# Optimization experiments

Measured on AMD Instinct MI355X. Metric: run time of the kernel, lower is better.

## Reference

```python
import jax, jax.numpy as jnp
import numpy as np

NR, NS, TAU, GW = 32, 64, 0.1, 0.5
NEG = jnp.float32(-1e30)

def _nrm(x):
    return x / jnp.maximum(jnp.linalg.norm(x, axis=-1, keepdims=True), 1e-12)

def _pair_loss(fb, ub, am, nm, ra, rp, rn):
    # fb [HW,D] features, ub [HW] uncertainty, am/nm [HW] bool anchor(=pos)/neg masks,
    # ra/rp/rn [HW] uniform random scores standing in for torch.randperm.
    def sel(mask, r, k):  # random subset of size k from mask (invalid slots flagged)
        _, idx = jax.lax.top_k(jnp.where(mask, r, NEG), k)
        return idx, mask[idx]
    def hard(mask, r):  # randperm[:2*Ns] then topk Ns by uncertainty
        cidx, cval = sel(mask, r, 2 * NS)
        _, t = jax.lax.top_k(jnp.where(cval, ub[cidx], NEG), NS)
        return cidx[t], cval[t]
    aidx, aval = sel(am, ra, NR)
    pidx, pval = hard(am, rp)
    nidx, nval = hard(nm, rn)
    q  = _nrm(fb[aidx])   # [NR,D]
    P  = _nrm(fb[pidx])   # [NS,D]
    Ng = _nrm(fb[nidx])   # [NS,D]
    pw = pval.astype(fb.dtype)[:, None]
    nw = nval.astype(fb.dtype)[:, None]
    p = (jnp.exp(P @ q.T / TAU) * pw).sum(0)   # [NR]
    n = (jnp.exp(Ng @ q.T / TAU) * nw).sum(0)  # [NR]
    inc = (am.sum() >= 1) & (nm.sum() >= 1)
    p = p + (1.0 - inc.astype(p.dtype))  # safe when excluded
    per = -jnp.log(p / (p + n + 1e-8))
    af = aval.astype(per.dtype)
    bl = (per * af).sum() / jnp.maximum(af.sum(), 1.0)
    return jnp.where(inc, bl, 0.0), inc

def _forward(feat, labels, prob_ori, prob_aug, unc, r_anc, r_pos, r_neg,
             w1, b1, gamma, beta, w2, b2):
    B, D, H, W = feat.shape
    # proj: 1x1 conv -> BN (training stats) -> relu -> 1x1 conv
    x = jnp.einsum('bdhw,ed->behw', feat, w1) + b1[None, :, None, None]
    mu = x.mean((0, 2, 3), keepdims=True)
    var = x.var((0, 2, 3), keepdims=True)
    x = gamma[None, :, None, None] * (x - mu) / jnp.sqrt(var + 1e-5) + beta[None, :, None, None]
    x = jax.nn.relu(x)
    proj = jnp.einsum('bdhw,ed->behw', x, w2) + b2[None, :, None, None]

    rel = prob_ori.argmax(1) == prob_aug.argmax(1)
    diff = unc > 0.5
    valid = (rel & diff).reshape(B, -1)
    lab = labels.reshape(B, -1)
    f = proj.transpose(0, 2, 3, 1).reshape(B, -1, D)
    uf = unc.reshape(B, -1)
    m1 = valid & (lab == 1)
    m0 = valid & (lab == 0)

    # ---- local loss: classes (1 vs 0) and (0 vs 1) ----
    anc = jnp.stack([m1, m0], 1)  # [B,2,HW]
    neg = jnp.stack([m0, m1], 1)
    pair = jax.vmap(jax.vmap(_pair_loss, in_axes=(None, None, 0, 0, 0, 0, 0)),
                    in_axes=(0, 0, 0, 0, 0, 0, 0))
    bl, inc = pair(f, uf, anc, neg, r_anc, r_pos, r_neg)
    l_local = bl.sum() / jnp.maximum(inc.sum(), 1)

    # ---- global loss with sequential memory bank (bank starts empty) ----
    fgf = m1.astype(f.dtype); bgf = m0.astype(f.dtype)
    cf = fgf.sum(1); cb = bgf.sum(1)
    m_fg = (f * fgf[..., None]).sum(1) / jnp.maximum(cf, 1.0)[:, None]
    m_bg = (f * bgf[..., None]).sum(1) / jnp.maximum(cb, 1.0)[:, None]
    vg = (cf >= 1) & (cb >= 1)
    qf, qb = _nrm(m_fg), _nrm(m_bg)
    # bank content at step b: prototypes of valid j <= b (detached)
    M = ((jnp.arange(B)[None, :] <= jnp.arange(B)[:, None]) & vg[None, :]).astype(f.dtype)  # [b,j]
    Sf = jnp.exp(jax.lax.stop_gradient(qb) @ qf.T / TAU)  # [j,b]
    Sb = jnp.exp(jax.lax.stop_gradient(qf) @ qb.T / TAU)
    nf = jnp.einsum('jb,bj->b', Sf, M)
    nb = jnp.einsum('jb,bj->b', Sb, M)
    pf = jnp.exp((qf * qf).sum(-1) / TAU)
    pb = jnp.exp((qb * qb).sum(-1) / TAU)
    lg = -jnp.log(pf / (pf + nf + 1e-8)) - jnp.log(pb / (pb + nb + 1e-8))
    l_global = (vg.astype(f.dtype) * lg).sum() / jnp.maximum(vg.sum(), 1)

    return l_local + GW * l_global, l_local, l_global

def setup_inputs() -> dict:
    key = jax.random.key(0)
    ks = jax.random.split(key, 16)
    B, D, H, W = 4, 256, 128, 128
    HW = H * W
    return {
        'feat': jax.random.normal(ks[0], (B, D, H, W), jnp.float32),
        'labels': jax.random.randint(ks[1], (B, H, W), 0, 2, jnp.int32),
        'prob_ori': jax.random.uniform(ks[2], (B, 2, H, W), jnp.float32),
        'prob_aug': jax.random.uniform(ks[3], (B, 2, H, W), jnp.float32),
        'unc': jax.random.uniform(ks[4], (B, H, W), jnp.float32),
        'r_anc': jax.random.uniform(ks[5], (B, 2, HW), jnp.float32),
        'r_pos': jax.random.uniform(ks[6], (B, 2, HW), jnp.float32),
        'r_neg': jax.random.uniform(ks[7], (B, 2, HW), jnp.float32),
        'w1': jax.random.normal(ks[8], (D, D), jnp.float32) * 0.05,
        'b1': jnp.zeros((D,), jnp.float32),
        'gamma': jnp.ones((D,), jnp.float32),
        'beta': jnp.zeros((D,), jnp.float32),
        'w2': jax.random.normal(ks[9], (D, D), jnp.float32) * 0.05,
        'b2': jnp.zeros((D,), jnp.float32),
    }

def reference(feat, labels, prob_ori, prob_aug, unc, r_anc, r_pos, r_neg,
              w1, b1, gamma, beta, w2, b2):
    return _forward(feat, labels, prob_ori, prob_aug, unc, r_anc, r_pos, r_neg,
                    w1, b1, gamma, beta, w2, b2)
```

## Files before the change

### kernel.cpp

```cpp
#include <hip/hip_runtime.h>
#include <hip/hip_bf16.h>
#include <float.h>
#include <math.h>

#define HW 16384
#define NBATCH 4
#define DIM 256
#define NEGV (-1e30f)
#define NPP 160

#define OFF_CHAN_SUM 0
#define OFF_CHAN_SQ  1024
#define OFF_MEAN     2048
#define OFF_ISTD     3072
#define OFF_S1       4096
#define OFF_S0       8192
#define OFF_CF       12288
#define OFF_CB       12304
#define OFF_BL       12320
#define OFF_INCF     12352
#define OFF_PPCNT    12416
#define OFF_QBUF     16384
#define OFF_BCNT     24576
#define OFF_MCLS     40960
#define OFF_SELIDX   303104
#define OFF_SELW     308224
#define OFF_ROWS     313344
#define OFF_W1T      1624064
#define OFF_RAW      1886208
#define OFF_CKEYS_XL 68995072
#define WS_NEED_FAST 68995072ull
#define WS_NEED_XL   72140800ull

#define NSEL 24

__device__ __forceinline__ unsigned f2mono(float f) {
  unsigned u = __float_as_uint(f);
  return (u & 0x80000000u) ? ~u : (u | 0x80000000u);
}

__device__ __forceinline__ void sort_desc(unsigned long long* sk, int* si, int n, int tid) {
  for (int ksz = 2; ksz <= n; ksz <<= 1) {
    for (int j = ksz >> 1; j > 0; j >>= 1) {
      __syncthreads();
      if (tid < n) {
        int ixj = tid ^ j;
        if (ixj > tid) {
          unsigned long long a = sk[tid], b = sk[ixj];
          bool up = (tid & ksz) == 0;
          if (up ? (a < b) : (a > b)) {
            sk[tid] = b; sk[ixj] = a;
            int t2 = si[tid]; si[tid] = si[ixj]; si[ixj] = t2;
          }
        }
      }
    }
  }
  __syncthreads();
}

__global__ __launch_bounds__(256) void k_maskc2(
    const float* __restrict__ po, const float* __restrict__ pa,
    const float* __restrict__ unc, const int* __restrict__ lab,
    const float* __restrict__ r_anc, const float* __restrict__ r_pos,
    const float* __restrict__ r_neg, const float* __restrict__ w1,
    int* __restrict__ mcls, int* __restrict__ bcnt,
    unsigned long long* __restrict__ ckeys, float* __restrict__ w1T,
    float* __restrict__ chanSum, float* __restrict__ chanSq,
    float* __restrict__ S1, float* __restrict__ S0,
    int* __restrict__ ppcnt) {
  __shared__ int lcnt[24];
  int tid = threadIdx.x;
  int g = blockIdx.x * 256 + tid;
  int b = g >> 14;
  int lb = blockIdx.x & 63;
  int i = g & (HW - 1);
  if (tid < 24) lcnt[tid] = 0;
  __syncthreads();
  float o0 = po[(size_t)(b*2+0)*HW + i];
  float o1 = po[(size_t)(b*2+1)*HW + i];
  float a0 = pa[(size_t)(b*2+0)*HW + i];
  float a1 = pa[(size_t)(b*2+1)*HW + i];
  bool rel = ((o1 > o0) == (a1 > a0));
  bool valid = rel && (unc[g] > 0.5f);
  int l = lab[g];
  int cls = valid ? ((l == 1) ? 1 : 2) : 0;
  mcls[g] = cls;
  int t0 = 0, t1 = 0, t2 = 0, loc0 = 0, loc1 = 0, loc2 = 0;
  unsigned long long k0 = 0, k1 = 0, k2 = 0;
  if (cls) {
    int co = cls - 1;
    unsigned idxf = (unsigned)(16383 - i);
    t0 = (b*2 + co)*3 + 0;
    t1 = (b*2 + co)*3 + 1;
    t2 = (b*2 + (1 - co))*3 + 2;
    k0 = ((unsigned long long)f2mono(r_anc[(size_t)(b*2 + co)*HW + i]) << 14) | idxf;
    k1 = ((unsigned long long)f2mono(r_pos[(size_t)(b*2 + co)*HW + i]) << 14) | idxf;
    k2 = ((unsigned long long)f2mono(r_neg[(size_t)(b*2 + (1 - co))*HW + i]) << 14) | idxf;
    loc0 = atomicAdd(&lcnt[t0], 1);
    loc1 = atomicAdd(&lcnt[t1], 1);
    loc2 = atomicAdd(&lcnt[t2], 1);
  }
  __syncthreads();
  if (tid < 24 && (tid / 6) == b)
    bcnt[tid*64 + lb] = lcnt[tid];
  if (cls) {
    ckeys[(size_t)t0*HW + lb*256 + loc0] = k0;
    ckeys[(size_t)t1*HW + lb*256 + loc1] = k1;
    ckeys[(size_t)t2*HW + lb*256 + loc2] = k2;
  }
  if (blockIdx.x < 16) {
    int d0 = blockIdx.x * 16;
    float v[16];
    #pragma unroll
    for (int j = 0; j < 16; ++j) v[j] = w1[(size_t)tid*DIM + d0 + j];
    #pragma unroll
    for (int j = 0; j < 16; ++j) w1T[(size_t)(d0 + j)*DIM + tid] = v[j];
  }
  if (blockIdx.x == 16) { chanSum[tid] = 0.f; chanSq[tid] = 0.f; }
  if (blockIdx.x == 17) {
    #pragma unroll
    for (int j = 0; j < 4; ++j) S1[j*256 + tid] = 0.f;
  }
  if (blockIdx.x == 18) {
    #pragma unroll
    for (int j = 0; j < 4; ++j) S0[j*256 + tid] = 0.f;
  }
  if (blockIdx.x == 19 && tid == 0) *ppcnt = 0;
}

__device__ void selc_body(const int* __restrict__ bcnt,
                          const unsigned long long* __restrict__ ckeys,
                          const float* __restrict__ unc,
                          int* __restrict__ selIdx, float* __restrict__ selW,
                          int* __restrict__ cf, int* __restrict__ cb,
                          int task, int tid, char* sh) {
  unsigned long long* sk = (unsigned long long*)sh;
  int* si    = (int*)(sh + 1024);
  int* cIdx  = (int*)(sh + 1536);
  int* hist  = (int*)(sh + 2048);
  int* sufs  = (int*)(sh + 3072);
  int* sbcnt = (int*)(sh + 4096);
  unsigned char* cVal = (unsigned char*)(sh + 4352);
  int* scal  = (int*)(sh + 4480);

  int pair = task / 3, which = task % 3;
  int b = pair >> 1, c = pair & 1;
  const unsigned long long* keys = ckeys + (size_t)task * HW;
  if (tid < 64) sbcnt[tid] = bcnt[task*64 + tid];
  __syncthreads();
  if (tid == 0) { int s = 0; for (int i2 = 0; i2 < 64; ++i2) s += sbcnt[i2]; scal[3] = s; }
  __syncthreads();
  int cnt = scal[3];
  if (which == 0 && tid == 0) { if (c == 0) cf[b] = cnt; else cb[b] = cnt; }
  int K1 = (which == 0) ? 32 : 128;
  int outBase = pair*NPP + (which == 0 ? 0 : (which == 1 ? 32 : 96));

  int mseg = tid >> 2;
  int msub = tid & 3;
  int mcnt = sbcnt[mseg];
  const unsigned long long* mkeys = keys + mseg*256;

  unsigned long long pref = 0;
  if (cnt > K1) {
    const int shifts[6]  = {38, 30, 22, 14, 6, 0};
    const int bitsArr[6] = { 8,  8,  8,  8, 8, 6};
    int k = K1;
    for (int p = 0; p < 6; ++p) {
      int shift = shifts[p], nbits = bitsArr[p], nb = 1 << nbits;
      hist[tid] = 0;
      __syncthreads();
      for (int pos = msub; pos < mcnt; pos += 4) {
        unsigned long long key = mkeys[pos];
        if ((key >> (shift + nbits)) == pref)
          atomicAdd(&hist[(int)((key >> shift) & (nb - 1))], 1);
      }
      __syncthreads();
      if (tid < nb) sufs[tid] = hist[tid];
      __syncthreads();
      for (int off = 1; off < nb; off <<= 1) {
        int add = 0;
        if (tid < nb && tid + off < nb) add = sufs[tid + off];
        __syncthreads();
        if (tid < nb) sufs[tid] += add;
        __syncthreads();
      }
      if (tid < nb) {
        int sthis = sufs[tid];
        int snext = (tid + 1 < nb) ? sufs[tid + 1] : 0;
        if (sthis >= k && snext < k) { scal[0] = tid; scal[1] = k - snext; }
      }
      __syncthreads();
      pref = (pref << nbits) | (unsigned)scal[0];
      k = scal[1];
      __syncthreads();
    }
  }

  if (tid == 0) scal[2] = 0;
  __syncthreads();
  for (int pos = msub; pos < mcnt; pos += 4) {
    unsigned long long key = mkeys[pos];
    if (key >= pref) {
      int p2 = atomicAdd(&scal[2], 1);
      if (p2 < 128) { sk[p2] = key; si[p2] = 16383 - (int)(key & 16383); }
    }
  }
  __syncthreads();
  int gcnt = scal[2];
  if (tid < K1 && tid >= gcnt) { sk[tid] = 0ull; si[tid] = 0; }

  sort_desc(sk, si, K1, tid);

  if (which == 0) {
    if (tid < 32) {
      selIdx[outBase + tid] = si[tid];
      selW[outBase + tid]   = (sk[tid] != 0ull) ? 1.f : 0.f;
    }
    return;
  }

  if (tid < 128) {
    cIdx[tid] = si[tid];
    cVal[tid] = (sk[tid] != 0ull) ? 1 : 0;
  }
  __syncthreads();
  if (tid < 128) {
    float u2 = cVal[tid] ? unc[(size_t)b*HW + cIdx[tid]] : NEGV;
    sk[tid] = ((unsigned long long)f2mono(u2) << 7) | (unsigned)(127 - tid);
    si[tid] = tid;
  }
  sort_desc(sk, si, 128, tid);
  if (tid < 64) {
    int t = si[tid];
    selIdx[outBase + tid] = cIdx[t];
    selW[outBase + tid]   = cVal[t] ? 1.f : 0.f;
  }
}

__global__ __launch_bounds__(256) void k_selc2(
    const int* __restrict__ bcnt, const unsigned long long* __restrict__ ckeys,
    const float* __restrict__ unc,
    int* __restrict__ selIdx, float* __restrict__ selW,
    int* __restrict__ cf, int* __restrict__ cb) {
  __shared__ __align__(16) char sh[4608];
  selc_body(bcnt, ckeys, unc, selIdx, selW, cf, cb, blockIdx.x, threadIdx.x, sh);
}

#define BK 32
#define LDA 132

__device__ void mm8_body(
    const float* __restrict__ feat, const float* __restrict__ w1T,
    const int* __restrict__ mcls,
    float* __restrict__ chanSum, float* __restrict__ chanSq,
    float* __restrict__ rawout, int bid, int tid, float* smem) {
  float* As = smem;
  float* Bs = smem + BK*LDA;
  int ct = bid & 1;
  int rt = bid >> 1;
  int b  = rt >> 7;
  int i0 = (rt & 127) << 7;
  int c0 = ct << 7;
  int tx = tid & 15, ty = tid >> 4;
  float acc[8][8];
  #pragma unroll
  for (int r = 0; r < 8; ++r)
    #pragma unroll
    for (int c = 0; c < 8; ++c) acc[r][c] = 0.f;

  for (int kc = 0; kc < 8; ++kc) {
    int d0 = kc * BK;
    #pragma unroll
    for (int it = 0; it < 4; ++it) {
      int e = it*1024 + tid*4;
      int k = e >> 7, r = e & 127;
      float4 v = *(const float4*)&feat[((size_t)(b*DIM + d0 + k))*HW + i0 + r];
      *(float4*)&As[k*LDA + r] = v;
    }
    #pragma unroll
    for (int it = 0; it < 4; ++it) {
      int e = it*1024 + tid*4;
      int k = e >> 7, c = e & 127;
      float4 v = *(const float4*)&w1T[(size_t)(d0 + k)*DIM + c0 + c];
      *(float4*)&Bs[k*LDA + c] = v;
    }
    __syncthreads();
    #pragma unroll
    for (int k = 0; k < BK; ++k) {
      float4 a0 = *(const float4*)&As[k*LDA + ty*4];
      float4 a1 = *(const float4*)&As[k*LDA + 64 + ty*4];
      float4 b0 = *(const float4*)&Bs[k*LDA + tx*4];
      float4 b1 = *(const float4*)&Bs[k*LDA + 64 + tx*4];
      float ar[8] = {a0.x,a0.y,a0.z,a0.w, a1.x,a1.y,a1.z,a1.w};
      float bc[8] = {b0.x,b0.y,b0.z,b0.w, b1.x,b1.y,b1.z,b1.w};
      #pragma unroll
      for (int r = 0; r < 8; ++r)
        #pragma unroll
        for (int c = 0; c < 8; ++c)
          acc[r][c] += ar[r]*bc[c];
    }
    __syncthreads();
  }

  float* pS = smem;
  float* pQ = smem + 2048;
  #pragma unroll
  for (int c = 0; c < 8; ++c) {
    int lcol = (c < 4) ? (tx*4 + c) : (64 + tx*4 + (c - 4));
    float s = 0.f, q = 0.f;
    #pragma unroll
    for (int r = 0; r < 8; ++r) { float v = acc[r][c]; s += v; q += v*v; }
    pS[ty*128 + lcol] = s;
    pQ[ty*128 + lcol] = q;
  }
  __syncthreads();
  if (tid < 128) {
    float s = 0.f, q = 0.f;
    #pragma unroll
    for (int t2 = 0; t2 < 16; ++t2) { s += pS[t2*128 + tid]; q += pQ[t2*128 + tid]; }
    atomicAdd(&chanSum[c0 + tid], s);
    atomicAdd(&chanSq[c0 + tid],  q);
  }

  #pragma unroll
  for (int r = 0; r < 8; ++r) {
    int lrow = (r < 4) ? (ty*4 + r) : (64 + ty*4 + (r - 4));
    int g = rt*128 + lrow;
    if (mcls[g] != 0) {
      float4 lo; lo.x = acc[r][0]; lo.y = acc[r][1]; lo.z = acc[r][2]; lo.w = acc[r][3];
      float4 hi; hi.x = acc[r][4]; hi.y = acc[r][5]; hi.z = acc[r][6]; hi.w = acc[r][7];
      *(float4*)&rawout[(size_t)g*DIM + c0 + tx*4]      = lo;
      *(float4*)&rawout[(size_t)g*DIM + c0 + 64 + tx*4] = hi;
    }
  }
}

__global__ __launch_bounds__(256) void k_mmsel(
    const float* __restrict__ feat, const float* __restrict__ w1T,
    const int* __restrict__ mcls,
    float* __restrict__ chanSum, float* __restrict__ chanSq,
    float* __restrict__ rawout,
    const int* __restrict__ bcnt, const unsigned long long* __restrict__ ckeys,
    const float* __restrict__ unc,
    int* __restrict__ selIdx, float* __restrict__ selW,
    int* __restrict__ cf, int* __restrict__ cb, int nSel) {
  __shared__ __align__(16) float smem[2*BK*LDA];
  int bid = blockIdx.x;
  if (bid < nSel)
    selc_body(bcnt, ckeys, unc, selIdx, selW, cf, cb, bid, threadIdx.x, (char*)smem);
  else
    mm8_body(feat, w1T, mcls, chanSum, chanSq, rawout, bid - nSel, threadIdx.x, smem);
}

__global__ __launch_bounds__(256) void k_post(
    const float* __restrict__ raw, const int* __restrict__ mcls,
    const float* __restrict__ chanSum, const float* __restrict__ chanSq,
    const float* __restrict__ gamma, const float* __restrict__ beta,
    const float* __restrict__ w2, const float* __restrict__ b2,
    const int* __restrict__ selIdx, const float* __restrict__ selW,
    float* __restrict__ S1, float* __restrict__ S0,
    float* __restrict__ rows) {
  __shared__ __align__(16) float sh[2048];
  const float nconst = (float)(NBATCH * HW);
  int tid = threadIdx.x;

  if (blockIdx.x < 256) {
    float* p1 = sh;
    float* p2 = sh + 1024;
    int w = tid >> 6, lane = tid & 63;
    int p0 = blockIdx.x << 8;
    int b = p0 >> 14;
    int ch = lane*4;
    float4 G = *(const float4*)&gamma[ch];
    float4 Bt = *(const float4*)&beta[ch];
    float4 CS = *(const float4*)&chanSum[ch];
    float4 CQ = *(const float4*)&chanSq[ch];
    float m0 = CS.x/nconst, m1 = CS.y/nconst, m2 = CS.z/nconst, m3 = CS.w/nconst;
    float v0 = CQ.x/nconst - m0*m0, v1 = CQ.y/nconst - m1*m1;
    float v2 = CQ.z/nconst - m2*m2, v3 = CQ.w/nconst - m3*m3;
    float i0 = 1.0f/sqrtf(v0 + 1e-5f), i1 = 1.0f/sqrtf(v1 + 1e-5f);
    float i2 = 1.0f/sqrtf(v2 + 1e-5f), i3 = 1.0f/sqrtf(v3 + 1e-5f);
    float A0 = G.x*i0, A1 = G.y*i1, A2 = G.z*i2, A3 = G.w*i3;
    float s1[4] = {0,0,0,0}, s0[4] = {0,0,0,0};
    int g0 = p0 + w*64;
    for (int t = 0; t < 64; ++t) {
      int g = g0 + t;
      int cls = mcls[g];
      if (cls == 0) continue;
      float4 v = *(const float4*)&raw[(size_t)g*DIM + ch];
      float r0 = A0*(v.x - m0) + Bt.x; r0 = r0 > 0.f ? r0 : 0.f;
      float r1 = A1*(v.y - m1) + Bt.y; r1 = r1 > 0.f ? r1 : 0.f;
      float r2 = A2*(v.z - m2) + Bt.z; r2 = r2 > 0.f ? r2 : 0.f;
      float r3 = A3*(v.w - m3) + Bt.w; r3 = r3 > 0.f ? r3 : 0.f;
      if (cls == 1) { s1[0]+=r0; s1[1]+=r1; s1[2]+=r2; s1[3]+=r3; }
      else          { s0[0]+=r0; s0[1]+=r1; s0[2]+=r2; s0[3]+=r3; }
    }
    #pragma unroll
    for (int j = 0; j < 4; ++j) {
      p1[w*256 + ch + j] = s1[j];
      p2[w*256 + ch + j] = s0[j];
    }
    __syncthreads();
    float a = p1[tid] + p1[256+tid] + p1[512+tid] + p1[768+tid];
    float d = p2[tid] + p2[256+tid] + p2[512+tid] + p2[768+tid];
    atomicAdd(&S1[b*DIM + tid], a);
    atomicAdd(&S0[b*DIM + tid], d);
  } else {
    float* rl  = sh;
    float* red = sh + 1024;
    int blk = blockIdx.x - 256;
    int slot0 = blk * 4;
    int pair = slot0 / NPP;
    int b = pair >> 1;
    int e = tid;
    float m = chanSum[e] / nconst;
    float v = chanSq[e] / nconst - m*m;
    float istd = 1.0f / sqrtf(v + 1e-5f);
    float A = gamma[e]*istd;
    float Bt = beta[e];
    bool ok[4];
    #pragma unroll
    for (int s = 0; s < 4; ++s) {
      int slot = slot0 + s;
      ok[s] = (selW[slot] != 0.f);
      float rv = 0.f;
      if (ok[s]) {
        int i = selIdx[slot];
        float acc = raw[((size_t)b*HW + i)*DIM + e];
        float bn = A*(acc - m) + Bt;
        rv = bn > 0.f ? bn : 0.f;
      }
      rl[s*256 + e] = rv;
    }
    __syncthreads();
    float b2e = b2[e];
    float pj[4] = {b2e, b2e, b2e, b2e};
    const float4* w4 = (const float4*)&w2[(size_t)e*DIM];
    #pragma unroll 8
    for (int d4 = 0; d4 < DIM/4; ++d4) {
      float4 w = w4[d4];
      #pragma unroll
      for (int s = 0; s < 4; ++s) {
        float4 a = *(const float4*)&rl[s*256 + d4*4];
        pj[s] += a.x*w.x + a.y*w.y + a.z*w.z + a.w*w.w;
      }
    }
    #pragma unroll
    for (int s = 0; s < 4; ++s) red[s*256 + e] = pj[s]*pj[s];
    __syncthreads();
    for (int off = 128; off > 0; off >>= 1) {
      if (e < off) {
        #pragma unroll
        for (int s = 0; s < 4; ++s) red[s*256 + e] += red[s*256 + e + off];
      }
      __syncthreads();
    }
    #pragma unroll
    for (int s = 0; s < 4; ++s) {
      float sc = 1.f / fmaxf(sqrtf(red[s*256]), 1e-12f);
      rows[(size_t)(slot0 + s)*DIM + e] = ok[s] ? pj[s]*sc : 0.f;
    }
  }
}

__device__ void pair_body(
    const float* __restrict__ rows, const float* __restrict__ selW,
    const int* __restrict__ cf, const int* __restrict__ cb,
    float* __restrict__ BL, float* __restrict__ INCF, int pair, int tid) {
  __shared__ float q[32*257];
  __shared__ float pacc[256], nacc[256];
  __shared__ float red[64];
  int b = pair >> 1, c = pair & 1;
  for (int l = tid; l < 32*DIM; l += 256) {
    int r = l >> 8, d = l & 255;
    q[r*257 + d] = rows[((size_t)pair*NPP + r)*DIM + d];
  }
  __syncthreads();
  int g = tid >> 5, r = tid & 31;
  float ap = 0.f, an = 0.f;
  for (int so = 0; so < 8; ++so) {
    int s = so*8 + g;
    const float* Pr = &rows[((size_t)pair*NPP + 32 + s)*DIM];
    const float* Nr = &rows[((size_t)pair*NPP + 96 + s)*DIM];
    float dp = 0.f, dn = 0.f;
    for (int d = 0; d < DIM; ++d) {
      float qv = q[r*257 + d];
      dp += Pr[d]*qv;
      dn += Nr[d]*qv;
    }
    ap += expf(dp*10.f) * selW[pair*NPP + 32 + s];
    an += expf(dn*10.f) * selW[pair*NPP + 96 + s];
  }
  pacc[tid] = ap; nacc[tid] = an;
  __syncthreads();
  if (tid < 32) {
    float p = 0.f, n = 0.f;
    for (int gg = 0; gg < 8; ++gg) { p += pacc[gg*32 + tid]; n += nacc[gg*32 + tid]; }
    int amC = (c == 0) ? cf[b] : cb[b];
    int nmC = (c == 0) ? cb[b] : cf[b];
    bool inc = (amC >= 1) && (nmC >= 1);
    if (!inc) p += 1.f;
    float per = -logf(p / (p + n + 1e-8f));
    float af = selW[pair*NPP + tid];
    red[tid]      = per*af;
    red[32 + tid] = af;
  }
  __syncthreads();
  if (tid == 0) {
    float s = 0.f, sa = 0.f;
    for (int rr = 0; rr < 32; ++rr) { s += red[rr]; sa += red[32+rr]; }
    int amC = (c == 0) ? cf[b] : cb[b];
    int nmC = (c == 0) ? cb[b] : cf[b];
    bool inc = (amC >= 1) && (nmC >= 1);
    float bl = s / fmaxf(sa, 1.f);
    BL[pair]   = inc ? bl : 0.f;
    INCF[pair] = inc ? 1.f : 0.f;
  }
}

__device__ void proto_body(
    const float* __restrict__ S1, const float* __restrict__ S0,
    const int* __restrict__ cf, const int* __restrict__ cb,
    const float* __restrict__ w2, const float* __restrict__ b2,
    float* __restrict__ qbuf, int idx, int l) {
  int b = idx >> 1, side = idx & 1;
  const float* S = (side == 0) ? &S1[b*DIM] : &S0[b*DIM];
  float cnt = (float)((side == 0) ? cf[b] : cb[b]);
  float m[4]; float n2p = 0.f;
  #pragma unroll
  for (int k = 0; k < 4; ++k) {
    int e = l + 64*k;
    float acc = 0.f;
    const float* w2r = &w2[(size_t)e*DIM];
    for (int d = 0; d < DIM; ++d) acc += S[d]*w2r[d];
    float mv = (acc + cnt*b2[e]) / fmaxf(cnt, 1.f);
    m[k] = mv; n2p += mv*mv;
  }
  #pragma unroll
  for (int off = 32; off > 0; off >>= 1) n2p += __shfl_down(n2p, off, 64);
  float n2 = __shfl(n2p, 0, 64);
  float sc = 1.f / fmaxf(sqrtf(n2), 1e-12f);
  #pragma unroll
  for (int k = 0; k < 4; ++k)
    qbuf[(size_t)(side*4 + b)*DIM + l + 64*k] = m[k]*sc;
}

__device__ void glob_body(
    const float* __restrict__ qbuf,
    const int* __restrict__ cf, const int* __restrict__ cb,
    const float* __restrict__ BL, const float* __restrict__ INCF,
    float* __restrict__ out, int l) {
  float qf[4][4], qb[4][4];
  #pragma unroll
  for (int b = 0; b < 4; ++b)
    #pragma unroll
    for (int k = 0; k < 4; ++k) {
      qf[b][k] = qbuf[(size_t)b*DIM + l + 64*k];
      qb[b][k] = qbuf[(size_t)(4 + b)*DIM + l + 64*k];
    }
  float pd[24];
  #pragma unroll
  for (int j = 0; j < 4; ++j)
    #pragma unroll
    for (int b = 0; b < 4; ++b) {
      float s = 0.f;
      #pragma unroll
      for (int k = 0; k < 4; ++k) s += qb[j][k]*qf[b][k];
      pd[j*4 + b] = s;
    }
  #pragma unroll
  for (int b = 0; b < 4; ++b) {
    float s1 = 0.f, s2 = 0.f;
    #pragma unroll
    for (int k = 0; k < 4; ++k) { s1 += qf[b][k]*qf[b][k]; s2 += qb[b][k]*qb[b][k]; }
    pd[16 + b] = s1; pd[20 + b] = s2;
  }
  #pragma unroll
  for (int t = 0; t < 24; ++t)
    #pragma unroll
    for (int off = 32; off > 0; off >>= 1)
      pd[t] += __shfl_down(pd[t], off, 64);
  if (l == 0) {
    bool vg[4]; float vgs = 0.f;
    for (int b = 0; b < 4; ++b) {
      vg[b] = (cf[b] >= 1) && (cb[b] >= 1);
      if (vg[b]) vgs += 1.f;
    }
    float gsum = 0.f;
    for (int b = 0; b < 4; ++b) {
      float nf = 0.f, nb = 0.f;
      for (int j = 0; j <= b; ++j) if (vg[j]) {
        nf += expf(10.f*pd[j*4 + b]);
        nb += expf(10.f*pd[b*4 + j]);
      }
      float pf = expf(10.f*pd[16 + b]);
      float pb = expf(10.f*pd[20 + b]);
      float lg = -logf(pf/(pf + nf + 1e-8f)) - logf(pb/(pb + nb + 1e-8f));
      if (vg[b]) gsum += lg;
    }
    float l_global = gsum / fmaxf(vgs, 1.f);
    float bls = 0.f, incs = 0.f;
    for (int p = 0; p < 8; ++p) { bls += BL[p]; incs += INCF[p]; }
    float l_local = bls / fmaxf(incs, 1.f);
    out[0] = l_local + 0.5f*l_global;
    out[1] = l_local;
    out[2] = l_global;
  }
}

__global__ __launch_bounds__(256) void k_pp(
    const float* __restrict__ rows, const float* __restrict__ selW,
    const int* __restrict__ cf, const int* __restrict__ cb,
    float* __restrict__ BL, float* __restrict__ INCF,
    const float* __restrict__ S1, const float* __restrict__ S0,
    const float* __restrict__ w2, const float* __restrict__ b2,
    float* __restrict__ qbuf, int* __restrict__ ppcnt,
    float* __restrict__ out) {
  __shared__ int isLast;
  if (blockIdx.x < 8) {
    pair_body(rows, selW, cf, cb, BL, INCF, blockIdx.x, threadIdx.x);
  } else {
    if (threadIdx.x < 64)
      proto_body(S1, S0, cf, cb, w2, b2, qbuf, blockIdx.x - 8, threadIdx.x);
  }
  __syncthreads();
  __threadfence();
  if (threadIdx.x == 0) isLast = (atomicAdd(ppcnt, 1) == 15);
  __syncthreads();
  if (isLast) {
    __threadfence();
    if (threadIdx.x < 64)
      glob_body(qbuf, cf, cb, BL, INCF, out, threadIdx.x);
  }
}

__global__ void k_mask(const float* __restrict__ po, const float* __restrict__ pa,
                       const float* __restrict__ unc, const int* __restrict__ lab,
                       int* __restrict__ mcls, int* __restrict__ cf, int* __restrict__ cb) {
  int g = blockIdx.x * 256 + threadIdx.x;
  int b = g >> 14;
  int i = g & (HW - 1);
  float o0 = po[(size_t)(b*2+0)*HW + i];
  float o1 = po[(size_t)(b*2+1)*HW + i];
  float a0 = pa[(size_t)(b*2+0)*HW + i];
  float a1 = pa[(size_t)(b*2+1)*HW + i];
  bool rel = ((o1 > o0) == (a1 > a0));
  bool valid = rel && (unc[g] > 0.5f);
  int l = lab[g];
  int cls = valid ? ((l == 1) ? 1 : 2) : 0;
  mcls[g] = cls;
  if (cls == 1) atomicAdd(&cf[b], 1);
  if (cls == 2) atomicAdd(&cb[b], 1);
}

template<int MODE>
__global__ __launch_bounds__(256) void k_matmul(
    const float* __restrict__ feat, const float* __restrict__ w1,
    float* __restrict__ chanSum, float* __restrict__ chanSq,
    const float* __restrict__ meanr, const float* __restrict__ istd,
    const float* __restrict__ gamma, const float* __restrict__ beta,
    const int* __restrict__ mcls,
    float* __restrict__ S1, float* __restrict__ S0) {
  __shared__ __align__(16) float As[64*68];
  __shared__ __align__(16) float Bs[64*68];
  __shared__ float cA[64], cB[64];
  int tid = threadIdx.x;
  int rt = blockIdx.x;
  int ct = blockIdx.y;
  int b  = rt >> 8;
  int i0 = (rt & 255) << 6;
  int c0 = ct << 6;
  int tx = tid & 15, ty = tid >> 4;
  float acc[4][4] = {{0.f,0.f,0.f,0.f},{0.f,0.f,0.f,0.f},{0.f,0.f,0.f,0.f},{0.f,0.f,0.f,0.f}};
  for (int kc = 0; kc < 4; ++kc) {
    int d0 = kc << 6;
    #pragma unroll
    for (int it = 0; it < 4; ++it) {
      int k  = it*16 + (tid >> 4);
      int rq = tid & 15;
      float4 v = *(const float4*)&feat[((size_t)(b*DIM + d0 + k))*HW + i0 + rq*4];
      *(float4*)&As[k*68 + rq*4] = v;
    }
    #pragma unroll
    for (int it = 0; it < 4; ++it) {
      int col = it*16 + (tid >> 4);
      int kq  = tid & 15;
      float4 v = *(const float4*)&w1[(size_t)(c0 + col)*DIM + d0 + kq*4];
      Bs[(kq*4+0)*68 + col] = v.x;
      Bs[(kq*4+1)*68 + col] = v.y;
      Bs[(kq*4+2)*68 + col] = v.z;
      Bs[(kq*4+3)*68 + col] = v.w;
    }
    __syncthreads();
    #pragma unroll
    for (int k = 0; k < 64; ++k) {
      float4 av = *(const float4*)&As[k*68 + ty*4];
      float4 bv = *(const float4*)&Bs[k*68 + tx*4];
      float aa[4] = {av.x, av.y, av.z, av.w};
      float bb[4] = {bv.x, bv.y, bv.z, bv.w};
      #pragma unroll
      for (int rr = 0; rr < 4; ++rr)
        #pragma unroll
        for (int cc = 0; cc < 4; ++cc)
          acc[rr][cc] += aa[rr]*bb[cc];
    }
    __syncthreads();
  }
  if (tid < 64) { cA[tid] = 0.f; cB[tid] = 0.f; }
  __syncthreads();
  if (MODE == 0) {
    float s[4] = {0,0,0,0}, q[4] = {0,0,0,0};
    #pragma unroll
    for (int rr = 0; rr < 4; ++rr)
      #pragma unroll
      for (int cc = 0; cc < 4; ++cc) { float v = acc[rr][cc]; s[cc] += v; q[cc] += v*v; }
    #pragma unroll
    for (int cc = 0; cc < 4; ++cc) {
      atomicAdd(&cA[tx*4+cc], s[cc]);
      atomicAdd(&cB[tx*4+cc], q[cc]);
    }
    __syncthreads();
    if (tid < 64) {
      atomicAdd(&chanSum[c0 + tid], cA[tid]);
      atomicAdd(&chanSq[c0 + tid],  cB[tid]);
    }
  } else {
    float A[4], M[4], Bt[4];
    #pragma unroll
    for (int cc = 0; cc < 4; ++cc) {
      int c = c0 + tx*4 + cc;
      A[cc] = gamma[c]*istd[c]; M[cc] = meanr[c]; Bt[cc] = beta[c];
    }
    float s1[4] = {0,0,0,0}, s0[4] = {0,0,0,0};
    #pragma unroll
    for (int rr = 0; rr < 4; ++rr) {
      int g = rt*64 + ty*4 + rr;
      int cls = mcls[g];
      if (cls == 0) continue;
      #pragma unroll
      for (int cc = 0; cc < 4; ++cc) {
        float v = A[cc]*(acc[rr][cc] - M[cc]) + Bt[cc];
        v = v > 0.f ? v : 0.f;
        if (cls == 1) s1[cc] += v; else s0[cc] += v;
      }
    }
    #pragma unroll
    for (int cc = 0; cc < 4; ++cc) {
      atomicAdd(&cA[tx*4+cc], s1[cc]);
      atomicAdd(&cB[tx*4+cc], s0[cc]);
    }
    __syncthreads();
    if (tid < 64) {
      atomicAdd(&S1[b*DIM + c0 + tid], cA[tid]);
      atomicAdd(&S0[b*DIM + c0 + tid], cB[tid]);
    }
  }
}

__global__ void k_stats(const float* __restrict__ chanSum, const float* __restrict__ chanSq,
                        float* __restrict__ meanr, float* __restrict__ istd) {
  int e = threadIdx.x;
  const float n = (float)(NBATCH * HW);
  float m = chanSum[e] / n;
  float v = chanSq[e] / n - m*m;
  meanr[e] = m;
  istd[e]  = 1.0f / sqrtf(v + 1e-5f);
}

__global__ __launch_bounds__(256) void k_select(
    const int* __restrict__ mcls,
    const float* __restrict__ r_anc, const float* __restrict__ r_pos, const float* __restrict__ r_neg,
    const float* __restrict__ unc,
    int* __restrict__ selIdx, float* __restrict__ selW) {
  __shared__ int hist[256];
  __shared__ int sufs[256];
  __shared__ unsigned long long sk[128];
  __shared__ int si[128];
  __shared__ int cIdx[128];
  __shared__ unsigned char cVal[128];
  __shared__ int sh_bin, sh_k, gcnt;

  int tid  = threadIdx.x;
  int task = blockIdx.x;
  int pair = task / 3, which = task % 3;
  int b = pair >> 1, c = pair & 1;
  int wantA = (c == 0) ? 1 : 2;
  int want  = (which == 2) ? (3 - wantA) : wantA;
  const int* mc = mcls + (size_t)b * HW;
  const float* r = (which == 0) ? r_anc : (which == 1 ? r_pos : r_neg);
  r += (size_t)(b*2 + c) * HW;

  int K1 = (which == 0) ? 32 : 128;
  int outBase = pair*NPP + (which == 0 ? 0 : (which == 1 ? 32 : 96));

  const int shifts[6]  = {38, 30, 22, 14, 6, 0};
  const int bitsArr[6] = { 8,  8,  8,  8, 8, 6};
  unsigned long long pref = 0;
  int k = K1;
  for (int p = 0; p < 6; ++p) {
    int shift = shifts[p];
    int nbits = bitsArr[p];
    int nb = 1 << nbits;
    hist[tid] = 0;
    __syncthreads();
    int lastBin = -1, lc = 0;
    #pragma unroll 4
    for (int j = 0; j < 64; ++j) {
      int i = tid + j*256;
      float kv = (mc[i] == want) ? r[i] : NEGV;
      unsigned long long key = ((unsigned long long)f2mono(kv) << 14) | (unsigned)(16383 - i);
      if ((key >> (shift + nbits)) == pref) {
        int bin = (int)((key >> shift) & (nb - 1));
        if (bin == lastBin) { ++lc; }
        else {
          if (lastBin >= 0) atomicAdd(&hist[lastBin], lc);
          lastBin = bin; lc = 1;
        }
      }
    }
    if (lastBin >= 0) atomicAdd(&hist[lastBin], lc);
    __syncthreads();
    if (tid < nb) sufs[tid] = hist[tid];
    __syncthreads();
    for (int off = 1; off < nb; off <<= 1) {
      int add = 0;
      if (tid < nb && tid + off < nb) add = sufs[tid + off];
      __syncthreads();
      if (tid < nb) sufs[tid] += add;
      __syncthreads();
    }
    if (tid < nb) {
      int sthis = sufs[tid];
      int snext = (tid + 1 < nb) ? sufs[tid + 1] : 0;
      if (sthis >= k && snext < k) { sh_bin = tid; sh_k = k - snext; }
    }
    __syncthreads();
    pref = (pref << nbits) | (unsigned)sh_bin;
    k = sh_k;
    __syncthreads();
  }

  if (tid == 0) gcnt = 0;
  __syncthreads();
  #pragma unroll 4
  for (int j = 0; j < 64; ++j) {
    int i = tid + j*256;
    float kv = (mc[i] == want) ? r[i] : NEGV;
    unsigned long long key = ((unsigned long long)f2mono(kv) << 14) | (unsigned)(16383 - i);
    if (key >= pref) {
      int p2 = atomicAdd(&gcnt, 1);
      if (p2 < 128) { sk[p2] = key; si[p2] = i; }
    }
  }
  __syncthreads();
  if (tid < K1 && tid >= gcnt) { sk[tid] = 0ull; si[tid] = 0; }

  sort_desc(sk, si, K1, tid);

  if (which == 0) {
    if (tid < 32) {
      selIdx[outBase + tid] = si[tid];
      selW[outBase + tid]   = ((sk[tid] >> 14) >= 0x80000000ull) ? 1.f : 0.f;
    }
    return;
  }

  if (tid < 128) {
    cIdx[tid] = si[tid];
    cVal[tid] = ((sk[tid] >> 14) >= 0x80000000ull) ? 1 : 0;
  }
  __syncthreads();
  if (tid < 128) {
    float u2 = cVal[tid] ? unc[(size_t)b*HW + cIdx[tid]] : NEGV;
    sk[tid] = ((unsigned long long)f2mono(u2) << 7) | (unsigned)(127 - tid);
    si[tid] = tid;
  }
  sort_desc(sk, si, 128, tid);
  if (tid < 64) {
    int t = si[tid];
    selIdx[outBase + tid] = cIdx[t];
    selW[outBase + tid]   = cVal[t] ? 1.f : 0.f;
  }
}

__global__ __launch_bounds__(256) void k_rowproj(
    const float* __restrict__ feat, const float* __restrict__ w1, const float* __restrict__ w2,
    const float* __restrict__ b2, const float* __restrict__ gamma, const float* __restrict__ beta,
    const float* __restrict__ meanr, const float* __restrict__ istd,
    const int* __restrict__ selIdx, float* __restrict__ rows) {
  __shared__ __align__(16) float fr[DIM];
  __shared__ __align__(16) float rl[DIM];
  __shared__ float red[256];
  int slot = blockIdx.x;
  int pair = slot / NPP;
  int b = pair >> 1;
  int i = selIdx[slot];
  int e = threadIdx.x;
  fr[e] = feat[((size_t)(b*DIM + e))*HW + i];
  __syncthreads();
  float acc = 0.f;
  {
    const float4* f4 = (const float4*)fr;
    const float4* w4 = (const float4*)&w1[(size_t)e*DIM];
    #pragma unroll 8
    for (int d = 0; d < DIM/4; ++d) {
      float4 a = f4[d], w = w4[d];
      acc += a.x*w.x + a.y*w.y + a.z*w.z + a.w*w.w;
    }
  }
  float bn = gamma[e]*istd[e]*(acc - meanr[e]) + beta[e];
  rl[e] = bn > 0.f ? bn : 0.f;
  __syncthreads();
  float pj = b2[e];
  {
    const float4* f4 = (const float4*)rl;
    const float4* w4 = (const float4*)&w2[(size_t)e*DIM];
    #pragma unroll 8
    for (int d = 0; d < DIM/4; ++d) {
      float4 a = f4[d], w = w4[d];
      pj += a.x*w.x + a.y*w.y + a.z*w.z + a.w*w.w;
    }
  }
  red[e] = pj*pj;
  __syncthreads();
  for (int off = 128; off > 0; off >>= 1) {
    if (e < off) red[e] += red[e+off];
    __syncthreads();
  }
  float sc = 1.f / fmaxf(sqrtf(red[0]), 1e-12f);
  rows[(size_t)slot*DIM + e] = pj * sc;
}

__global__ __launch_bounds__(256) void k_pair(
    const float* __restrict__ rows, const float* __restrict__ selW,
    const int* __restrict__ cf, const int* __restrict__ cb,
    float* __restrict__ BL, float* __restrict__ INCF) {
  pair_body(rows, selW, cf, cb, BL, INCF, blockIdx.x, threadIdx.x);
}

__global__ __launch_bounds__(64) void k_proto(
    const float* __restrict__ S1, const float* __restrict__ S0,
    const int* __restrict__ cf, const int* __restrict__ cb,
    const float* __restrict__ w2, const float* __restrict__ b2,
    float* __restrict__ qbuf) {
  proto_body(S1, S0, cf, cb, w2, b2, qbuf, blockIdx.x, threadIdx.x);
}

__global__ __launch_bounds__(64) void k_glob(
    const float* __restrict__ qbuf,
    const int* __restrict__ cf, const int* __restrict__ cb,
    const float* __restrict__ BL, const float* __restrict__ INCF,
    float* __restrict__ out) {
  glob_body(qbuf, cf, cb, BL, INCF, out, threadIdx.x);
}

extern "C" void kernel_launch(void* const* d_in, const int* in_sizes, int n_in,
                              void* d_out, int out_size, void* d_ws, size_t ws_size,
                              hipStream_t stream) {
  const float* feat     = (const float*)d_in[0];
  const int*   labels   = (const int*)  d_in[1];
  const float* prob_ori = (const float*)d_in[2];
  const float* prob_aug = (const float*)d_in[3];
  const float* unc      = (const float*)d_in[4];
  const float* r_anc    = (const float*)d_in[5];
  const float* r_pos    = (const float*)d_in[6];
  const float* r_neg    = (const float*)d_in[7];
  const float* w1       = (const float*)d_in[8];
  const float* gamma    = (const float*)d_in[10];
  const float* beta     = (const float*)d_in[11];
  const float* w2       = (const float*)d_in[12];
  const float* b2       = (const float*)d_in[13];

  char* ws = (char*)d_ws;
  float* chanSum = (float*)(ws + OFF_CHAN_SUM);
  float* chanSq  = (float*)(ws + OFF_CHAN_SQ);
  float* meanr   = (float*)(ws + OFF_MEAN);
  float* istd    = (float*)(ws + OFF_ISTD);
  float* S1      = (float*)(ws + OFF_S1);
  float* S0      = (float*)(ws + OFF_S0);
  int*   cf      = (int*)  (ws + OFF_CF);
  int*   cb      = (int*)  (ws + OFF_CB);
  float* BLp     = (float*)(ws + OFF_BL);
  float* INCp    = (float*)(ws + OFF_INCF);
  int*   ppcnt   = (int*)  (ws + OFF_PPCNT);
  float* qbuf    = (float*)(ws + OFF_QBUF);
  int*   bcnt    = (int*)  (ws + OFF_BCNT);
  int*   mclsp   = (int*)  (ws + OFF_MCLS);
  int*   selIdx  = (int*)  (ws + OFF_SELIDX);
  float* selW    = (float*)(ws + OFF_SELW);
  float* rowsbuf = (float*)(ws + OFF_ROWS);
  float* w1T     = (float*)(ws + OFF_W1T);
  float* rawbuf  = (float*)(ws + OFF_RAW);

  if (ws_size >= WS_NEED_FAST) {
    bool xl = (ws_size >= WS_NEED_XL);
    unsigned long long* ckeys = (unsigned long long*)(ws + (xl ? OFF_CKEYS_XL : OFF_RAW));

    k_maskc2<<<256, 256, 0, stream>>>(prob_ori, prob_aug, unc, labels,
                                      r_anc, r_pos, r_neg, w1,
                                      mclsp, bcnt, ckeys, w1T,
                                      chanSum, chanSq, S1, S0, ppcnt);
    if (xl) {
      k_mmsel<<<1024 + NSEL, 256, 0, stream>>>(feat, w1T, mclsp, chanSum, chanSq, rawbuf,
                                               bcnt, ckeys, unc, selIdx, selW, cf, cb, NSEL);
    } else {
      k_selc2<<<24, 256, 0, stream>>>(bcnt, ckeys, unc, selIdx, selW, cf, cb);
      k_mmsel<<<1024, 256, 0, stream>>>(feat, w1T, mclsp, chanSum, chanSq, rawbuf,
                                        bcnt, ckeys, unc, selIdx, selW, cf, cb, 0);
    }

    k_post<<<576, 256, 0, stream>>>(rawbuf, mclsp, chanSum, chanSq, gamma, beta,
                                    w2, b2, selIdx, selW, S1, S0, rowsbuf);

    k_pp<<<16, 256, 0, stream>>>(rowsbuf, selW, cf, cb, BLp, INCp,
                                 S1, S0, w2, b2, qbuf, ppcnt, (float*)d_out);
  } else {
    hipMemsetAsync(d_ws, 0, 16384, stream);
    k_mask<<<256, 256, 0, stream>>>(prob_ori, prob_aug, unc, labels, mclsp, cf, cb);
    dim3 gmm(1024, 4);
    k_matmul<0><<<gmm, 256, 0, stream>>>(feat, w1, chanSum, chanSq,
                                         meanr, istd, gamma, beta, mclsp, S1, S0);
    k_stats<<<1, 256, 0, stream>>>(chanSum, chanSq, meanr, istd);
    k_matmul<1><<<gmm, 256, 0, stream>>>(feat, w1, chanSum, chanSq,
                                         meanr, istd, gamma, beta, mclsp, S1, S0);
    k_select<<<24, 256, 0, stream>>>(mclsp, r_anc, r_pos, r_neg, unc, selIdx, selW);
    k_rowproj<<<1280, 256, 0, stream>>>(feat, w1, w2, b2, gamma, beta, meanr, istd,
                                        selIdx, rowsbuf);
    k_pair<<<8, 256, 0, stream>>>(rowsbuf, selW, cf, cb, BLp, INCp);
    k_proto<<<8, 64, 0, stream>>>(S1, S0, cf, cb, w2, b2, qbuf);
    k_glob<<<1, 64, 0, stream>>>(qbuf, cf, cb, BLp, INCp, (float*)d_out);
  }
}
```

Measured before the change: 298.3 us.

## Fuse post and pair/proto kernels into one launch with atomic-counter barrier

Merges the k_post and k_pp launches into a single k_tail kernel. The trailing 16 blocks spin on a global atomic counter until all 576 post blocks have finished, then run the pair/proto and final global reduction. The goal is to remove one kernel launch and the inter-kernel gap. It also changes the matmul shared-memory padding from 132 to 128, which can bring back LDS bank conflicts. The spin-wait relies on the post blocks being scheduled before the waiting blocks, which is a deadlock risk if they are not co-resident.

```diff
diff --git a/kernel.cpp b/kernel.cpp
--- a/kernel.cpp
+++ b/kernel.cpp
@@ -33,6 +33,8 @@
 #define WS_NEED_XL   72140800ull
 
 #define NSEL 24
+#define NPOST 576
+#define NTAIL (NPOST + 16)
 
 __device__ __forceinline__ unsigned f2mono(float f) {
   unsigned u = __float_as_uint(f);
@@ -126,7 +128,7 @@
     #pragma unroll
     for (int j = 0; j < 4; ++j) S0[j*256 + tid] = 0.f;
   }
-  if (blockIdx.x == 19 && tid == 0) *ppcnt = 0;
+  if (blockIdx.x == 19 && tid < 2) ppcnt[tid] = 0;
 }
 
 __device__ void selc_body(const int* __restrict__ bcnt,
@@ -248,7 +250,7 @@
 }
 
 #define BK 32
-#define LDA 132
+#define LDA 128
 
 __device__ void mm8_body(
     const float* __restrict__ feat, const float* __restrict__ w1T,
@@ -353,23 +355,22 @@
     mm8_body(feat, w1T, mcls, chanSum, chanSq, rawout, bid - nSel, threadIdx.x, smem);
 }
 
-__global__ __launch_bounds__(256) void k_post(
+__device__ void post_body(
     const float* __restrict__ raw, const int* __restrict__ mcls,
     const float* __restrict__ chanSum, const float* __restrict__ chanSq,
     const float* __restrict__ gamma, const float* __restrict__ beta,
     const float* __restrict__ w2, const float* __restrict__ b2,
     const int* __restrict__ selIdx, const float* __restrict__ selW,
     float* __restrict__ S1, float* __restrict__ S0,
-    float* __restrict__ rows) {
-  __shared__ __align__(16) float sh[2048];
+    float* __restrict__ rows, int pblk, int tid, char* shc) {
+  float* sh = (float*)shc;
   const float nconst = (float)(NBATCH * HW);
-  int tid = threadIdx.x;
-
-  if (blockIdx.x < 256) {
+
+  if (pblk < 256) {
     float* p1 = sh;
     float* p2 = sh + 1024;
     int w = tid >> 6, lane = tid & 63;
-    int p0 = blockIdx.x << 8;
+    int p0 = pblk << 8;
     int b = p0 >> 14;
     int ch = lane*4;
     float4 G = *(const float4*)&gamma[ch];
@@ -409,7 +410,7 @@
   } else {
     float* rl  = sh;
     float* red = sh + 1024;
-    int blk = blockIdx.x - 256;
+    int blk = pblk - 256;
     int slot0 = blk * 4;
     int pair = slot0 / NPP;
     int b = pair >> 1;
@@ -467,10 +468,12 @@
 __device__ void pair_body(
     const float* __restrict__ rows, const float* __restrict__ selW,
     const int* __restrict__ cf, const int* __restrict__ cb,
-    float* __restrict__ BL, float* __restrict__ INCF, int pair, int tid) {
-  __shared__ float q[32*257];
-  __shared__ float pacc[256], nacc[256];
-  __shared__ float red[64];
+    float* __restrict__ BL, float* __restrict__ INCF, int pair, int tid,
+    char* shc) {
+  float* q    = (float*)shc;
+  float* pacc = q + 32*257;
+  float* nacc = pacc + 256;
+  float* red  = nacc + 256;
   int b = pair >> 1, c = pair & 1;
   for (int l = tid; l < 32*DIM; l += 256) {
     int r = l >> 8, d = l & 255;
@@ -609,29 +612,50 @@
   }
 }
 
-__global__ __launch_bounds__(256) void k_pp(
-    const float* __restrict__ rows, const float* __restrict__ selW,
+__global__ __launch_bounds__(256) void k_tail(
+    const float* __restrict__ raw, const int* __restrict__ mcls,
+    const float* __restrict__ chanSum, const float* __restrict__ chanSq,
+    const float* __restrict__ gamma, const float* __restrict__ beta,
+    const float* __restrict__ w2, const float* __restrict__ b2,
+    const int* __restrict__ selIdx, const float* __restrict__ selW,
+    float* __restrict__ S1, float* __restrict__ S0,
+    float* __restrict__ rows,
     const int* __restrict__ cf, const int* __restrict__ cb,
     float* __restrict__ BL, float* __restrict__ INCF,
-    const float* __restrict__ S1, const float* __restrict__ S0,
-    const float* __restrict__ w2, const float* __restrict__ b2,
-    float* __restrict__ qbuf, int* __restrict__ ppcnt,
+    float* __restrict__ qbuf, int* __restrict__ cnts,
     float* __restrict__ out) {
+  __shared__ __align__(16) char shb[35328];
   __shared__ int isLast;
-  if (blockIdx.x < 8) {
-    pair_body(rows, selW, cf, cb, BL, INCF, blockIdx.x, threadIdx.x);
+  int tid = threadIdx.x;
+  int bid = blockIdx.x;
+  if (bid < NPOST) {
+    post_body(raw, mcls, chanSum, chanSq, gamma, beta, w2, b2,
+              selIdx, selW, S1, S0, rows, bid, tid, shb);
+    __syncthreads();
+    __threadfence();
+    if (tid == 0) atomicAdd(&cnts[0], 1);
+    return;
+  }
+  if (tid == 0) {
+    while (atomicAdd(&cnts[0], 0) < NPOST) __builtin_amdgcn_s_sleep(32);
+  }
+  __syncthreads();
+  __threadfence();
+  int t = bid - NPOST;
+  if (t < 8) {
+    pair_body(rows, selW, cf, cb, BL, INCF, t, tid, shb);
   } else {
-    if (threadIdx.x < 64)
-      proto_body(S1, S0, cf, cb, w2, b2, qbuf, blockIdx.x - 8, threadIdx.x);
+    if (tid < 64)
+      proto_body(S1, S0, cf, cb, w2, b2, qbuf, t - 8, tid);
   }
   __syncthreads();
   __threadfence();
-  if (threadIdx.x == 0) isLast = (atomicAdd(ppcnt, 1) == 15);
+  if (tid == 0) isLast = (atomicAdd(&cnts[1], 1) == 15);
   __syncthreads();
   if (isLast) {
     __threadfence();
-    if (threadIdx.x < 64)
-      glob_body(qbuf, cf, cb, BL, INCF, out, threadIdx.x);
+    if (tid < 64)
+      glob_body(qbuf, cf, cb, BL, INCF, out, tid);
   }
 }
 
@@ -936,7 +960,8 @@
     const float* __restrict__ rows, const float* __restrict__ selW,
     const int* __restrict__ cf, const int* __restrict__ cb,
     float* __restrict__ BL, float* __restrict__ INCF) {
-  pair_body(rows, selW, cf, cb, BL, INCF, blockIdx.x, threadIdx.x);
+  __shared__ __align__(16) char shb[35328];
+  pair_body(rows, selW, cf, cb, BL, INCF, blockIdx.x, threadIdx.x, shb);
 }
 
 __global__ __launch_bounds__(64) void k_proto(
@@ -1010,11 +1035,9 @@
                                         bcnt, ckeys, unc, selIdx, selW, cf, cb, 0);
     }
 
-    k_post<<<576, 256, 0, stream>>>(rawbuf, mclsp, chanSum, chanSq, gamma, beta,
-                                    w2, b2, selIdx, selW, S1, S0, rowsbuf);
-
-    k_pp<<<16, 256, 0, stream>>>(rowsbuf, selW, cf, cb, BLp, INCp,
-                                 S1, S0, w2, b2, qbuf, ppcnt, (float*)d_out);
+    k_tail<<<NTAIL, 256, 0, stream>>>(rawbuf, mclsp, chanSum, chanSq, gamma, beta,
+                                      w2, b2, selIdx, selW, S1, S0, rowsbuf,
+                                      cf, cb, BLp, INCp, qbuf, ppcnt, (float*)d_out);
   } else {
     hipMemsetAsync(d_ws, 0, 16384, stream);
     k_mask<<<256, 256, 0, stream>>>(prob_ori, prob_aug, unc, labels, mclsp, cf, cb);
```

Result: slower. 332.7 us (+11.5%).
